# Performance work log

Measured on AMD Instinct MI355X. Metric: run time of the kernel, lower is better.

## Reference

```python
import jax, jax.numpy as jnp
import numpy as np

DIM = 2048
N_HEADS = 32
N_KV_HEADS = 8
HEAD_DIM = 64
N_REP = N_HEADS // N_KV_HEADS
SEQ = 2048
BATCH = 1


def _llama3_scaled_rope(head_dim, end, base=10000.0, scale_factor=8):
    # matches executorch precompute_freqs_cis with use_scaled=True
    freqs = 1.0 / (base ** (np.arange(0, head_dim, 2)[: head_dim // 2] / head_dim))
    low_freq_factor, high_freq_factor, old_ctx = 1.0, 4.0, 8192.0
    low_wl = old_ctx / low_freq_factor
    high_wl = old_ctx / high_freq_factor
    wavelen = 2.0 * np.pi / freqs
    smooth = (old_ctx / wavelen - low_freq_factor) / (high_freq_factor - low_freq_factor)
    scaled = np.where(
        wavelen < high_wl,
        freqs,
        np.where(wavelen > low_wl, freqs / scale_factor,
                 (1.0 - smooth) * freqs / scale_factor + smooth * freqs),
    )
    t = np.arange(end, dtype=np.float64)
    ang = np.outer(t, scaled)
    return np.cos(ang).astype(np.float32), np.sin(ang).astype(np.float32)


def setup_inputs() -> dict:
    key = jax.random.key(0)
    kx, kq, kk, kv, ko = jax.random.split(key, 5)
    x = jax.random.normal(kx, (BATCH, SEQ, DIM), dtype=jnp.float32)
    sc = 0.02
    wq = jax.random.normal(kq, (N_HEADS * HEAD_DIM, DIM), dtype=jnp.float32) * sc
    wk = jax.random.normal(kk, (N_KV_HEADS * HEAD_DIM, DIM), dtype=jnp.float32) * sc
    wv = jax.random.normal(kv, (N_KV_HEADS * HEAD_DIM, DIM), dtype=jnp.float32) * sc
    wo = jax.random.normal(ko, (N_HEADS * HEAD_DIM, DIM), dtype=jnp.float32).T * sc
    cos, sin = _llama3_scaled_rope(HEAD_DIM, SEQ)
    return {"x": x, "freqs_cos": jnp.asarray(cos), "freqs_sin": jnp.asarray(sin),
            "wq": wq, "wk": wk, "wv": wv, "wo": wo}


def _apply_rotary(x, cos, sin):
    # x: [b, s, h, hd]; cos/sin: [s, hd//2]; interleaved-pair RoPE
    xr = x[..., 0::2]
    xi = x[..., 1::2]
    c = cos[None, :, None, :]
    s = sin[None, :, None, :]
    out_r = xr * c - xi * s
    out_i = xr * s + xi * c
    return jnp.stack([out_r, out_i], axis=-1).reshape(x.shape)


def reference(x, freqs_cos, freqs_sin, wq, wk, wv, wo):
    b, s, _ = x.shape
    q = (x @ wq.T).reshape(b, s, N_HEADS, HEAD_DIM)
    k = (x @ wk.T).reshape(b, s, N_KV_HEADS, HEAD_DIM)
    v = (x @ wv.T).reshape(b, s, N_KV_HEADS, HEAD_DIM)
    q = _apply_rotary(q, freqs_cos, freqs_sin)
    k = _apply_rotary(k, freqs_cos, freqs_sin)
    # [b, h, s, hd]
    q = q.transpose(0, 2, 1, 3)
    k = k.transpose(0, 2, 1, 3)
    v = v.transpose(0, 2, 1, 3)
    # GQA: repeat_interleave over head dim
    k = jnp.repeat(k, N_REP, axis=1)
    v = jnp.repeat(v, N_REP, axis=1)
    scale = 1.0 / jnp.sqrt(jnp.asarray(HEAD_DIM, dtype=x.dtype))
    scores = jnp.einsum("bhqd,bhkd->bhqk", q, k) * scale
    causal = jnp.tril(jnp.ones((s, s), dtype=bool))
    scores = jnp.where(causal[None, None], scores, jnp.finfo(scores.dtype).min)
    attn = jax.nn.softmax(scores, axis=-1)
    y = jnp.einsum("bhqk,bhkd->bhqd", attn, v)
    y = y.transpose(0, 2, 1, 3).reshape(b, s, N_HEADS * HEAD_DIM)
    return y @ wo.T
```

## Files before the change

kernel.cpp:

```cpp
#include <hip/hip_runtime.h>
#include <hip/hip_bf16.h>

typedef __attribute__((ext_vector_type(8))) __bf16 bf16x8;
typedef __attribute__((ext_vector_type(4))) __bf16 bf16x4;
typedef __attribute__((ext_vector_type(4))) float f32x4;

#define DIM 2048
#define SEQ 2048
#define NH 32
#define NKV 8
#define HD 64
#define QKVD 3072
#define KOFF 2048
#define VOFF 2560
#define KVDIM 512

__device__ __forceinline__ void gld16(const __bf16* g, __bf16* l) {
    __builtin_amdgcn_global_load_lds(
        (const __attribute__((address_space(1))) void*)g,
        (__attribute__((address_space(3))) void*)l, 16, 0, 0);
}

__global__ __launch_bounds__(256) void cvt_all(const float* __restrict__ x,
                                               const float* __restrict__ wq,
                                               const float* __restrict__ wk,
                                               const float* __restrict__ wv,
                                               const float* __restrict__ wo,
                                               __bf16* __restrict__ xb,
                                               __bf16* __restrict__ wqkvb,
                                               __bf16* __restrict__ wob) {
    const int i = blockIdx.x * blockDim.x + threadIdx.x;
    const int NX = SEQ * DIM / 4;
    const int NW = DIM * DIM / 4;
    const int NKV4 = KVDIM * DIM / 4;
    const float* src; __bf16* dst; int off;
    if (i < NX)                        { src = x;  dst = xb;    off = i; }
    else if (i < NX + NW)              { src = wq; dst = wqkvb; off = i - NX; }
    else if (i < NX + NW + NKV4)       { src = wk; dst = wqkvb + (size_t)KOFF * DIM; off = i - NX - NW; }
    else if (i < NX + NW + 2 * NKV4)   { src = wv; dst = wqkvb + (size_t)VOFF * DIM; off = i - NX - NW - NKV4; }
    else                               { src = wo; dst = wob;   off = i - NX - NW - 2 * NKV4; }
    float4 v = reinterpret_cast<const float4*>(src)[off];
    bf16x4 o;
    o[0] = (__bf16)v.x; o[1] = (__bf16)v.y; o[2] = (__bf16)v.z; o[3] = (__bf16)v.w;
    reinterpret_cast<bf16x4*>(dst)[off] = o;
}

template <typename OutT, bool ROPE>
__global__ __launch_bounds__(512, 6) void gemm_tn(const __bf16* __restrict__ A,
                                                  const __bf16* __restrict__ B,
                                                  OutT* __restrict__ C,
                                                  int M, int N, int K,
                                                  float scale, int scaleNlim,
                                                  const float* __restrict__ fc,
                                                  const float* __restrict__ fs,
                                                  __bf16* __restrict__ VTout) {
    __shared__ __align__(16) __bf16 As[2][2][128 * 32];
    __shared__ __align__(16) __bf16 Bs[2][2][64 * 32];
    const int tid = threadIdx.x;
    const int lane = tid & 63;
    const int w = tid >> 6;
    const int l15 = lane & 15, lhi = lane >> 4;
    const int mb = blockIdx.y * 128;
    const int nb = blockIdx.x * 64;
    const int wm = (w >> 1) * 32, wn = (w & 1) * 32;

    const int srow = lane >> 2, scol = (lane & 3) * 8;
    const __bf16* gA = A + (size_t)(mb + w * 16 + srow) * K + scol;
    const __bf16* gB = B + (size_t)(nb + (w & 3) * 16 + srow) * K + scol;
    const int bsub = w >> 2;

    auto stage = [&](int kk, int buf) {
#pragma unroll
        for (int s = 0; s < 2; ++s)
            gld16(gA + kk + s * 32, As[buf][s] + w * 512);
        gld16(gB + kk + bsub * 32, Bs[buf][bsub] + (w & 3) * 512);
    };

    stage(0, 0);
    __syncthreads();

    f32x4 acc[2][2] = {};
    int cur = 0;
    for (int kk = 0; kk < K; kk += 64, cur ^= 1) {
        if (kk + 64 < K) stage(kk + 64, cur ^ 1);
#pragma unroll
        for (int s = 0; s < 2; ++s) {
            bf16x8 a[2], b[2];
#pragma unroll
            for (int i = 0; i < 2; ++i)
                a[i] = *reinterpret_cast<const bf16x8*>(&As[cur][s][(wm + i * 16 + l15) * 32 + lhi * 8]);
#pragma unroll
            for (int j = 0; j < 2; ++j)
                b[j] = *reinterpret_cast<const bf16x8*>(&Bs[cur][s][(wn + j * 16 + l15) * 32 + lhi * 8]);
#pragma unroll
            for (int i = 0; i < 2; ++i)
#pragma unroll
                for (int j = 0; j < 2; ++j)
                    acc[i][j] = __builtin_amdgcn_mfma_f32_16x16x32_bf16(a[i], b[j], acc[i][j], 0, 0, 0);
        }
        __syncthreads();
    }

    const bool toVT = ROPE && (VTout != nullptr) && (nb >= VOFF);
    if (toVT) {
#pragma unroll
        for (int i = 0; i < 2; ++i)
#pragma unroll
            for (int j = 0; j < 2; ++j) {
                bf16x4 pv;
#pragma unroll
                for (int r = 0; r < 4; ++r) pv[r] = (__bf16)acc[i][j][r];
                const int colv = nb - VOFF + wn + j * 16 + l15;
                const int row0 = mb + wm + i * 16 + lhi * 4;
                *reinterpret_cast<bf16x4*>(VTout + (size_t)colv * M + row0) = pv;
            }
    } else {
        const float sc = (nb < scaleNlim) ? scale : 1.0f;
        const bool doRope = ROPE && (nb < VOFF);
#pragma unroll
        for (int i = 0; i < 2; ++i)
#pragma unroll
            for (int j = 0; j < 2; ++j)
#pragma unroll
                for (int r = 0; r < 4; ++r) {
                    float v = acc[i][j][r] * sc;
                    if (doRope) {
                        const int col = nb + wn + j * 16 + l15;
                        const int row = mb + wm + i * 16 + lhi * 4 + r;
                        const float vp = __shfl_xor(v, 1);
                        const int fi = (col & 63) >> 1;
                        const float cc = fc[row * 32 + fi];
                        const float ss = fs[row * 32 + fi];
                        v = (col & 1) ? (vp * ss + v * cc) : (v * cc - vp * ss);
                    }
                    C[(size_t)(mb + wm + i * 16 + lhi * 4 + r) * N + nb + wn + j * 16 + l15] = (OutT)v;
                }
    }
}

__global__ __launch_bounds__(128, 4) void attn_kernel(const __bf16* __restrict__ QKV,
                                                      const __bf16* __restrict__ VT,
                                                      __bf16* __restrict__ Y) {
    const int bx = blockIdx.x;
    const int t = 63 - (bx >> 5);
    const int h = bx & 31;
    const int kvh = h >> 2;
    const int tid = threadIdx.x;
    const int lane = tid & 63;
    const int w = tid >> 6;
    const int l15 = lane & 15, lhi = lane >> 4;

    __shared__ __align__(16) __bf16 Kl[64 * 64];
    __shared__ __align__(16) __bf16 Vl[64 * 64];
    __shared__ __align__(16) __bf16 Pl[2][16 * 64];

    const __bf16* Qp = QKV + h * HD;
    const __bf16* Kp = QKV + KOFF + kvh * HD;
    const __bf16* Vth = VT + (size_t)(kvh * HD) * SEQ;

    const int sr = lane >> 3;
    const int ksc = ((lane & 7) ^ sr) * 8;
    const int rswz = (l15 & 7);

    auto stage = [&](int jt) {
        const int kvb = jt * 64;
#pragma unroll
        for (int c = 0; c < 4; ++c) {
            const int row = w * 32 + c * 8;
            gld16(Kp + (size_t)(kvb + row + sr) * QKVD + ksc, &Kl[row * 64]);
            gld16(Vth + (size_t)(row + sr) * SEQ + kvb + ksc, &Vl[row * 64]);
        }
    };

    const int qb = t * 32;
    const int nkt = (t >> 1) + 1;
    const int qrow = qb + w * 16 + l15;

    const __bf16* qptr = Qp + (size_t)qrow * QKVD;
    bf16x8 qf0 = *reinterpret_cast<const bf16x8*>(qptr + lhi * 8);
    bf16x8 qf1 = *reinterpret_cast<const bf16x8*>(qptr + 32 + lhi * 8);

    bf16x8 ones1;
#pragma unroll
    for (int i = 0; i < 8; ++i) ones1[i] = (__bf16)1.0f;

    f32x4 o[4] = {};
    f32x4 oS = {};
    float mrun = -1e30f;

    const int pkey = (l15 & 7) << 1;

    for (int j = 0; j < nkt; ++j) {
        __syncthreads();
        stage(j);
        __syncthreads();

        f32x4 sacc[4];
        __builtin_amdgcn_s_setprio(1);
#pragma unroll
        for (int tt = 0; tt < 4; ++tt) {
            const int rb = (tt * 16 + l15) * 64;
            bf16x8 kf0 = *reinterpret_cast<const bf16x8*>(
                &Kl[rb + ((lhi ^ rswz) * 8)]);
            bf16x8 kf1 = *reinterpret_cast<const bf16x8*>(
                &Kl[rb + (((4 + lhi) ^ rswz) * 8)]);
            f32x4 z = {0.f, 0.f, 0.f, 0.f};
            z = __builtin_amdgcn_mfma_f32_16x16x32_bf16(kf0, qf0, z, 0, 0, 0);
            z = __builtin_amdgcn_mfma_f32_16x16x32_bf16(kf1, qf1, z, 0, 0, 0);
            sacc[tt] = z;
        }
        __builtin_amdgcn_s_setprio(0);

        if (j == nkt - 1) {
#pragma unroll
            for (int tt = 0; tt < 4; ++tt)
#pragma unroll
                for (int r = 0; r < 4; ++r) {
                    const int kv = j * 64 + tt * 16 + lhi * 4 + r;
                    if (kv > qrow) sacc[tt][r] = -1e30f;
                }
        }

        float mt[4];
#pragma unroll
        for (int tt = 0; tt < 4; ++tt)
            mt[tt] = fmaxf(fmaxf(sacc[tt][0], sacc[tt][1]),
                           fmaxf(sacc[tt][2], sacc[tt][3]));
        const float pm = fmaxf(fmaxf(mt[0], mt[1]), fmaxf(mt[2], mt[3]));

        if (!__all(pm - mrun <= 8.0f)) {
            float full = pm;
            full = fmaxf(full, __shfl_xor(full, 16));
            full = fmaxf(full, __shfl_xor(full, 32));
            const float mn = fmaxf(mrun, full);
            const float aa = exp2f(mrun - mn);
            mrun = mn;
            float ar[4];
#pragma unroll
            for (int r = 0; r < 4; ++r) ar[r] = __shfl(aa, lhi * 4 + r);
#pragma unroll
            for (int tt = 0; tt < 4; ++tt)
#pragma unroll
                for (int r = 0; r < 4; ++r) o[tt][r] *= ar[r];
#pragma unroll
            for (int r = 0; r < 4; ++r) oS[r] *= ar[r];
        }

#pragma unroll
        for (int tt = 0; tt < 4; ++tt) {
            bf16x4 pk;
#pragma unroll
            for (int r = 0; r < 4; ++r)
                pk[r] = (__bf16)exp2f(sacc[tt][r] - mrun);
            const int sw = (tt * 4 + lhi) ^ pkey;
            *reinterpret_cast<bf16x4*>(&Pl[w][l15 * 64 + sw * 4]) = pk;
        }

        bf16x8 pf0 = *reinterpret_cast<const bf16x8*>(
            &Pl[w][l15 * 64 + (((lhi * 2) ^ pkey) * 4)]);
        bf16x8 pf1 = *reinterpret_cast<const bf16x8*>(
            &Pl[w][l15 * 64 + (((8 + lhi * 2) ^ pkey) * 4)]);
        __builtin_amdgcn_s_setprio(1);
#pragma unroll
        for (int tt = 0; tt < 4; ++tt) {
            const int rb = (tt * 16 + l15) * 64;
            bf16x8 vf0 = *reinterpret_cast<const bf16x8*>(
                &Vl[rb + ((lhi ^ rswz) * 8)]);
            bf16x8 vf1 = *reinterpret_cast<const bf16x8*>(
                &Vl[rb + (((4 + lhi) ^ rswz) * 8)]);
            o[tt] = __builtin_amdgcn_mfma_f32_16x16x32_bf16(pf0, vf0, o[tt], 0, 0, 0);
            o[tt] = __builtin_amdgcn_mfma_f32_16x16x32_bf16(pf1, vf1, o[tt], 0, 0, 0);
        }
        oS = __builtin_amdgcn_mfma_f32_16x16x32_bf16(pf0, ones1, oS, 0, 0, 0);
        oS = __builtin_amdgcn_mfma_f32_16x16x32_bf16(pf1, ones1, oS, 0, 0, 0);
        __builtin_amdgcn_s_setprio(0);
    }

#pragma unroll
    for (int tt = 0; tt < 4; ++tt)
#pragma unroll
        for (int r = 0; r < 4; ++r) {
            const float val = o[tt][r] / oS[r];
            Y[(size_t)(qb + w * 16 + lhi * 4 + r) * DIM + h * HD + tt * 16 + l15] =
                (__bf16)val;
        }
}

extern "C" void kernel_launch(void* const* d_in, const int* in_sizes, int n_in,
                              void* d_out, int out_size, void* d_ws, size_t ws_size,
                              hipStream_t stream) {
    const float* x    = (const float*)d_in[0];
    const float* fcos = (const float*)d_in[1];
    const float* fsin = (const float*)d_in[2];
    const float* wq   = (const float*)d_in[3];
    const float* wk   = (const float*)d_in[4];
    const float* wv   = (const float*)d_in[5];
    const float* wo   = (const float*)d_in[6];
    float* out = (float*)d_out;

    __bf16* xb    = (__bf16*)d_ws;
    __bf16* wqkvb = xb + (size_t)SEQ * DIM;
    __bf16* wob   = wqkvb + (size_t)QKVD * DIM;
    __bf16* QKVb  = wob + (size_t)DIM * DIM;
    __bf16* Yb    = QKVb + (size_t)SEQ * QKVD;
    __bf16* VTb   = Yb + (size_t)SEQ * DIM;

    const int ncvt = (SEQ * DIM / 4) + 2 * (DIM * DIM / 4) + 2 * (KVDIM * DIM / 4);
    cvt_all<<<ncvt / 256, 256, 0, stream>>>(x, wq, wk, wv, wo, xb, wqkvb, wob);

    gemm_tn<__bf16, true><<<dim3(QKVD / 64, SEQ / 128), 512, 0, stream>>>(
        xb, wqkvb, QKVb, SEQ, QKVD, DIM, 0.125f * 1.4426950408889634f, KOFF,
        fcos, fsin, VTb);

    attn_kernel<<<dim3(2048), 128, 0, stream>>>(QKVb, VTb, Yb);

    gemm_tn<float, false><<<dim3(DIM / 64, SEQ / 128), 512, 0, stream>>>(
        Yb, wob, out, SEQ, DIM, DIM, 1.0f, 0, nullptr, nullptr, nullptr);
}
```

Before: 137.5 us.

## Split KV loop across two wave groups with 4-buffer prefetch and merge

The attention kernel now uses 512-thread blocks over 64-query tiles, with two groups of four waves each handling alternating KV tiles (split-K within the block). KV tiles are prefetched into a 4-slot shared ring one pair ahead, so there is one barrier per pair instead of two per tile. The two partial softmax states are merged through shared-memory scratch at the end. The intent is more parallelism per query tile and overlap of loads with compute. The cost is more LDS per block (about 80KB), a final merge step, and idle waves when the tile count is odd.

```diff
diff --git a/kernel.cpp b/kernel.cpp
--- a/kernel.cpp
+++ b/kernel.cpp
@@ -138,21 +138,23 @@
     }
 }
 
-__global__ __launch_bounds__(128, 4) void attn_kernel(const __bf16* __restrict__ QKV,
+__global__ __launch_bounds__(512, 2) void attn_kernel(const __bf16* __restrict__ QKV,
                                                       const __bf16* __restrict__ VT,
                                                       __bf16* __restrict__ Y) {
     const int bx = blockIdx.x;
-    const int t = 63 - (bx >> 5);
+    const int qt = 31 - (bx >> 5);
     const int h = bx & 31;
     const int kvh = h >> 2;
     const int tid = threadIdx.x;
     const int lane = tid & 63;
     const int w = tid >> 6;
+    const int grp = w >> 2;
+    const int sub = w & 3;
     const int l15 = lane & 15, lhi = lane >> 4;
 
-    __shared__ __align__(16) __bf16 Kl[64 * 64];
-    __shared__ __align__(16) __bf16 Vl[64 * 64];
-    __shared__ __align__(16) __bf16 Pl[2][16 * 64];
+    __shared__ __align__(16) __bf16 Kl[4][64 * 64];
+    __shared__ __align__(16) __bf16 Vl[4][64 * 64];
+    __shared__ __align__(16) __bf16 Pl[8][16 * 64];
 
     const __bf16* Qp = QKV + h * HD;
     const __bf16* Kp = QKV + KOFF + kvh * HD;
@@ -163,18 +165,18 @@
     const int rswz = (l15 & 7);
 
     auto stage = [&](int jt) {
+        const int buf = jt & 3;
         const int kvb = jt * 64;
 #pragma unroll
-        for (int c = 0; c < 4; ++c) {
-            const int row = w * 32 + c * 8;
-            gld16(Kp + (size_t)(kvb + row + sr) * QKVD + ksc, &Kl[row * 64]);
-            gld16(Vth + (size_t)(row + sr) * SEQ + kvb + ksc, &Vl[row * 64]);
+        for (int c = 0; c < 2; ++c) {
+            const int row = sub * 16 + c * 8;
+            gld16(Kp + (size_t)(kvb + row + sr) * QKVD + ksc, &Kl[buf][row * 64]);
+            gld16(Vth + (size_t)(row + sr) * SEQ + kvb + ksc, &Vl[buf][row * 64]);
         }
     };
 
-    const int qb = t * 32;
-    const int nkt = (t >> 1) + 1;
-    const int qrow = qb + w * 16 + l15;
+    const int qb = qt * 64;
+    const int qrow = qb + sub * 16 + l15;
 
     const __bf16* qptr = Qp + (size_t)qrow * QKVD;
     bf16x8 qf0 = *reinterpret_cast<const bf16x8*>(qptr + lhi * 8);
@@ -190,100 +192,139 @@
 
     const int pkey = (l15 & 7) << 1;
 
-    for (int j = 0; j < nkt; ++j) {
+    if (grp <= qt) stage(grp);
+    __syncthreads();
+
+    const int npair = (qt >> 1) + 1;
+    for (int jj = 0; jj < npair; ++jj) {
+        const int jnext = 2 * jj + 2 + grp;
+        if (jnext <= qt) stage(jnext);
+
+        const int jw = 2 * jj + grp;
+        if (jw <= qt) {
+            const __bf16* Kb = Kl[jw & 3];
+            const __bf16* Vb = Vl[jw & 3];
+
+            f32x4 sacc[4];
+            __builtin_amdgcn_s_setprio(1);
+#pragma unroll
+            for (int tt = 0; tt < 4; ++tt) {
+                const int rb = (tt * 16 + l15) * 64;
+                bf16x8 kf0 = *reinterpret_cast<const bf16x8*>(
+                    &Kb[rb + ((lhi ^ rswz) * 8)]);
+                bf16x8 kf1 = *reinterpret_cast<const bf16x8*>(
+                    &Kb[rb + (((4 + lhi) ^ rswz) * 8)]);
+                f32x4 z = {0.f, 0.f, 0.f, 0.f};
+                z = __builtin_amdgcn_mfma_f32_16x16x32_bf16(kf0, qf0, z, 0, 0, 0);
+                z = __builtin_amdgcn_mfma_f32_16x16x32_bf16(kf1, qf1, z, 0, 0, 0);
+                sacc[tt] = z;
+            }
+            __builtin_amdgcn_s_setprio(0);
+
+            if (jw == qt) {
+#pragma unroll
+                for (int tt = 0; tt < 4; ++tt)
+#pragma unroll
+                    for (int r = 0; r < 4; ++r) {
+                        const int kv = jw * 64 + tt * 16 + lhi * 4 + r;
+                        if (kv > qrow) sacc[tt][r] = -1e30f;
+                    }
+            }
+
+            float mt[4];
+#pragma unroll
+            for (int tt = 0; tt < 4; ++tt)
+                mt[tt] = fmaxf(fmaxf(sacc[tt][0], sacc[tt][1]),
+                               fmaxf(sacc[tt][2], sacc[tt][3]));
+            const float pm = fmaxf(fmaxf(mt[0], mt[1]), fmaxf(mt[2], mt[3]));
+
+            if (!__all(pm - mrun <= 8.0f)) {
+                float full = pm;
+                full = fmaxf(full, __shfl_xor(full, 16));
+                full = fmaxf(full, __shfl_xor(full, 32));
+                const float mn = fmaxf(mrun, full);
+                const float aa = exp2f(mrun - mn);
+                mrun = mn;
+                float ar[4];
+#pragma unroll
+                for (int r = 0; r < 4; ++r) ar[r] = __shfl(aa, lhi * 4 + r);
+#pragma unroll
+                for (int tt = 0; tt < 4; ++tt)
+#pragma unroll
+                    for (int r = 0; r < 4; ++r) o[tt][r] *= ar[r];
+#pragma unroll
+                for (int r = 0; r < 4; ++r) oS[r] *= ar[r];
+            }
+
+#pragma unroll
+            for (int tt = 0; tt < 4; ++tt) {
+                bf16x4 pk;
+#pragma unroll
+                for (int r = 0; r < 4; ++r)
+                    pk[r] = (__bf16)exp2f(sacc[tt][r] - mrun);
+                const int sw = (tt * 4 + lhi) ^ pkey;
+                *reinterpret_cast<bf16x4*>(&Pl[w][l15 * 64 + sw * 4]) = pk;
+            }
+
+            bf16x8 pf0 = *reinterpret_cast<const bf16x8*>(
+                &Pl[w][l15 * 64 + (((lhi * 2) ^ pkey) * 4)]);
+            bf16x8 pf1 = *reinterpret_cast<const bf16x8*>(
+                &Pl[w][l15 * 64 + (((8 + lhi * 2) ^ pkey) * 4)]);
+            __builtin_amdgcn_s_setprio(1);
+#pragma unroll
+            for (int tt = 0; tt < 4; ++tt) {
+                const int rb = (tt * 16 + l15) * 64;
+                bf16x8 vf0 = *reinterpret_cast<const bf16x8*>(
+                    &Vb[rb + ((lhi ^ rswz) * 8)]);
+                bf16x8 vf1 = *reinterpret_cast<const bf16x8*>(
+                    &Vb[rb + (((4 + lhi) ^ rswz) * 8)]);
+                o[tt] = __builtin_amdgcn_mfma_f32_16x16x32_bf16(pf0, vf0, o[tt], 0, 0, 0);
+                o[tt] = __builtin_amdgcn_mfma_f32_16x16x32_bf16(pf1, vf1, o[tt], 0, 0, 0);
+            }
+            oS = __builtin_amdgcn_mfma_f32_16x16x32_bf16(pf0, ones1, oS, 0, 0, 0);
+            oS = __builtin_amdgcn_mfma_f32_16x16x32_bf16(pf1, ones1, oS, 0, 0, 0);
+            __builtin_amdgcn_s_setprio(0);
+        }
+
         __syncthreads();
-        stage(j);
-        __syncthreads();
-
-        f32x4 sacc[4];
-        __builtin_amdgcn_s_setprio(1);
-#pragma unroll
-        for (int tt = 0; tt < 4; ++tt) {
-            const int rb = (tt * 16 + l15) * 64;
-            bf16x8 kf0 = *reinterpret_cast<const bf16x8*>(
-                &Kl[rb + ((lhi ^ rswz) * 8)]);
-            bf16x8 kf1 = *reinterpret_cast<const bf16x8*>(
-                &Kl[rb + (((4 + lhi) ^ rswz) * 8)]);
-            f32x4 z = {0.f, 0.f, 0.f, 0.f};
-            z = __builtin_amdgcn_mfma_f32_16x16x32_bf16(kf0, qf0, z, 0, 0, 0);
-            z = __builtin_amdgcn_mfma_f32_16x16x32_bf16(kf1, qf1, z, 0, 0, 0);
-            sacc[tt] = z;
+    }
+
+    float* o_scr = (float*)Kl;
+    float* m_scr = (float*)Vl;
+
+    if (grp == 1) {
+        float* dst = o_scr + ((size_t)(sub * 64 + lane)) * 20;
+#pragma unroll
+        for (int tt = 0; tt < 4; ++tt)
+#pragma unroll
+            for (int r = 0; r < 4; ++r) dst[tt * 4 + r] = o[tt][r];
+#pragma unroll
+        for (int r = 0; r < 4; ++r) dst[16 + r] = oS[r];
+        if (lhi == 0) m_scr[sub * 16 + l15] = mrun;
+    }
+    __syncthreads();
+    if (grp == 0) {
+        const float mB = m_scr[sub * 16 + l15];
+        const float mn = fmaxf(mrun, mB);
+        const float a0 = exp2f(mrun - mn);
+        const float a1 = exp2f(mB - mn);
+        const float* src = o_scr + ((size_t)(sub * 64 + lane)) * 20;
+        float A0[4], A1[4], den[4];
+#pragma unroll
+        for (int r = 0; r < 4; ++r) {
+            A0[r] = __shfl(a0, lhi * 4 + r);
+            A1[r] = __shfl(a1, lhi * 4 + r);
+            den[r] = oS[r] * A0[r] + src[16 + r] * A1[r];
         }
-        __builtin_amdgcn_s_setprio(0);
-
-        if (j == nkt - 1) {
-#pragma unroll
-            for (int tt = 0; tt < 4; ++tt)
-#pragma unroll
-                for (int r = 0; r < 4; ++r) {
-                    const int kv = j * 64 + tt * 16 + lhi * 4 + r;
-                    if (kv > qrow) sacc[tt][r] = -1e30f;
-                }
-        }
-
-        float mt[4];
 #pragma unroll
         for (int tt = 0; tt < 4; ++tt)
-            mt[tt] = fmaxf(fmaxf(sacc[tt][0], sacc[tt][1]),
-                           fmaxf(sacc[tt][2], sacc[tt][3]));
-        const float pm = fmaxf(fmaxf(mt[0], mt[1]), fmaxf(mt[2], mt[3]));
-
-        if (!__all(pm - mrun <= 8.0f)) {
-            float full = pm;
-            full = fmaxf(full, __shfl_xor(full, 16));
-            full = fmaxf(full, __shfl_xor(full, 32));
-            const float mn = fmaxf(mrun, full);
-            const float aa = exp2f(mrun - mn);
-            mrun = mn;
-            float ar[4];
-#pragma unroll
-            for (int r = 0; r < 4; ++r) ar[r] = __shfl(aa, lhi * 4 + r);
-#pragma unroll
-            for (int tt = 0; tt < 4; ++tt)
-#pragma unroll
-                for (int r = 0; r < 4; ++r) o[tt][r] *= ar[r];
-#pragma unroll
-            for (int r = 0; r < 4; ++r) oS[r] *= ar[r];
-        }
-
-#pragma unroll
-        for (int tt = 0; tt < 4; ++tt) {
-            bf16x4 pk;
-#pragma unroll
-            for (int r = 0; r < 4; ++r)
-                pk[r] = (__bf16)exp2f(sacc[tt][r] - mrun);
-            const int sw = (tt * 4 + lhi) ^ pkey;
-            *reinterpret_cast<bf16x4*>(&Pl[w][l15 * 64 + sw * 4]) = pk;
-        }
-
-        bf16x8 pf0 = *reinterpret_cast<const bf16x8*>(
-            &Pl[w][l15 * 64 + (((lhi * 2) ^ pkey) * 4)]);
-        bf16x8 pf1 = *reinterpret_cast<const bf16x8*>(
-            &Pl[w][l15 * 64 + (((8 + lhi * 2) ^ pkey) * 4)]);
-        __builtin_amdgcn_s_setprio(1);
-#pragma unroll
-        for (int tt = 0; tt < 4; ++tt) {
-            const int rb = (tt * 16 + l15) * 64;
-            bf16x8 vf0 = *reinterpret_cast<const bf16x8*>(
-                &Vl[rb + ((lhi ^ rswz) * 8)]);
-            bf16x8 vf1 = *reinterpret_cast<const bf16x8*>(
-                &Vl[rb + (((4 + lhi) ^ rswz) * 8)]);
-            o[tt] = __builtin_amdgcn_mfma_f32_16x16x32_bf16(pf0, vf0, o[tt], 0, 0, 0);
-            o[tt] = __builtin_amdgcn_mfma_f32_16x16x32_bf16(pf1, vf1, o[tt], 0, 0, 0);
-        }
-        oS = __builtin_amdgcn_mfma_f32_16x16x32_bf16(pf0, ones1, oS, 0, 0, 0);
-        oS = __builtin_amdgcn_mfma_f32_16x16x32_bf16(pf1, ones1, oS, 0, 0, 0);
-        __builtin_amdgcn_s_setprio(0);
-    }
-
-#pragma unroll
-    for (int tt = 0; tt < 4; ++tt)
-#pragma unroll
-        for (int r = 0; r < 4; ++r) {
-            const float val = o[tt][r] / oS[r];
-            Y[(size_t)(qb + w * 16 + lhi * 4 + r) * DIM + h * HD + tt * 16 + l15] =
-                (__bf16)val;
-        }
+#pragma unroll
+            for (int r = 0; r < 4; ++r) {
+                const float num = o[tt][r] * A0[r] + src[tt * 4 + r] * A1[r];
+                Y[(size_t)(qb + sub * 16 + lhi * 4 + r) * DIM + h * HD + tt * 16 + l15] =
+                    (__bf16)(num / den[r]);
+            }
+    }
 }
 
 extern "C" void kernel_launch(void* const* d_in, const int* in_sizes, int n_in,
@@ -312,7 +353,7 @@
         xb, wqkvb, QKVb, SEQ, QKVD, DIM, 0.125f * 1.4426950408889634f, KOFF,
         fcos, fsin, VTb);
 
-    attn_kernel<<<dim3(2048), 128, 0, stream>>>(QKVb, VTb, Yb);
+    attn_kernel<<<dim3(1024), 512, 0, stream>>>(QKVb, VTb, Yb);
 
     gemm_tn<float, false><<<dim3(DIM / 64, SEQ / 128), 512, 0, stream>>>(
         Yb, wob, out, SEQ, DIM, DIM, 1.0f, 0, nullptr, nullptr, nullptr);
```

Measured after the change: 133.7 us. 1.03x faster.
